# Performance work log

Measured on AMD Instinct MI355X. Metric: run time of the kernel, lower is better.

The kernel has to match this reference:

```python
import jax, jax.numpy as jnp
import numpy as np

B, N, D, C = 32, 8192, 256, 1000  # batch, nodes, dim (dim_original == dim_attention), num_class


def setup_inputs() -> dict:
    key = jax.random.key(0)
    ks = jax.random.split(key, 6)
    s = 1.0 / np.sqrt(D)
    return {
        "atom": jax.random.normal(ks[0], (B, N, D), dtype=jnp.float32),
        "obj": jax.random.normal(ks[1], (B, D), dtype=jnp.float32),
        "W": jax.random.uniform(ks[2], (D, D), jnp.float32, -s, s),        # nn.Linear(D, D, bias=False).weight
        "A": jax.random.uniform(ks[3], (1, 2 * D), jnp.float32, -1.0 / np.sqrt(2 * D), 1.0 / np.sqrt(2 * D)),  # nn.Linear(2D, 1, bias=False).weight
        "CW": jax.random.uniform(ks[4], (C, 2 * D), jnp.float32, -1.0 / np.sqrt(2 * D), 1.0 / np.sqrt(2 * D)),  # classifier weight
        "CB": jax.random.uniform(ks[5], (C,), jnp.float32, -1.0 / np.sqrt(2 * D), 1.0 / np.sqrt(2 * D)),        # classifier bias
    }


def reference(atom, obj, W, A, CW, CB):
    # a1 = w(atom): [B, N, D]; o1 = w(obj): [B, D]
    a1 = jnp.einsum("bnd,kd->bnk", atom, W)
    o1 = obj @ W.T
    # att = Linear_a(cat(a1, broadcast(o1)))  == a1 @ A1 + o1 @ A2 (no concat materialized)
    A1, A2 = A[0, :D], A[0, D:]
    att = a1 @ A1 + (o1 @ A2)[:, None]          # [B, N] attention scores (no softmax)
    # message_a2o = att_weights.bmm(a1).squeeze(): [B, D]
    msg = jnp.einsum("bn,bnd->bd", att, a1)
    # inte == 'concat': classifier(cat(o1, msg))
    preds = jnp.concatenate([o1, msg], axis=-1) @ CW.T + CB  # [B, C]
    return preds
```

## Files before the change

### kernel.cpp

```cpp
#include <hip/hip_runtime.h>

#define DD 256
#define BB 32
#define NN 8192
#define CC 1000
#define SUBS 32
#define CACHED_B 16

typedef float f4 __attribute__((ext_vector_type(4)));

__device__ __forceinline__ f4 ntload(const float* p) {
    return __builtin_nontemporal_load((const f4*)p);
}

template <int CTRL>
__device__ __forceinline__ float dpp_ror_add(float s) {
    int r = __builtin_amdgcn_update_dpp(0, __float_as_int(s), CTRL, 0xF, 0xF, true);
    return s + __int_as_float(r);
}
__device__ __forceinline__ float rowsum16(float s) {
    s = dpp_ror_add<0x121>(s);
    s = dpp_ror_add<0x122>(s);
    s = dpp_ror_add<0x124>(s);
    s = dpp_ror_add<0x128>(s);
    return s;
}

__global__ __launch_bounds__(256) void k_prep(const float* __restrict__ W,
                                              const float* __restrict__ A,
                                              const float* __restrict__ obj,
                                              float* __restrict__ v1,
                                              float* __restrict__ c) {
    int b = blockIdx.x, t = threadIdx.x;
    int q  = t >> 6;
    int cs = (t & 63) * 4;
    __shared__ float s1[4][DD], s2[4][DD];
    __shared__ float sc[4];
    f4 a1 = {0.f, 0.f, 0.f, 0.f}, a2 = a1;
#pragma unroll 8
    for (int k = q; k < DD; k += 4) {
        f4 w = *(const f4*)(W + (size_t)k * DD + cs);
        a1 += A[k] * w;
        a2 += A[DD + k] * w;
    }
    *(f4*)&s1[q][cs] = a1;
    *(f4*)&s2[q][cs] = a2;
    __syncthreads();
    float vv1 = s1[0][t] + s1[1][t] + s1[2][t] + s1[3][t];
    float vv2 = s2[0][t] + s2[1][t] + s2[2][t] + s2[3][t];
    if (b == 0) v1[t] = vv1;
    float p = vv2 * obj[(size_t)b * DD + t];
    p = rowsum16(p);
    p += __shfl_xor(p, 16, 64);
    p += __shfl_xor(p, 32, 64);
    if ((t & 63) == 0) sc[t >> 6] = p;
    __syncthreads();
    if (t == 0) c[b] = sc[0] + sc[1] + sc[2] + sc[3];
}

template <bool NT>
__device__ __forceinline__ void atom_loop(const float* __restrict__ p,
                                          const float4& w0, const float4& w1,
                                          const float4& w2, const float4& w3,
                                          float cb,
                                          f4& A0, f4& A1, f4& A2, f4& A3) {
#pragma unroll 4
    for (int g = 0; g < 16; ++g) {
        f4 x0 = NT ? ntload(p)       : *(const f4*)(p);
        f4 x1 = NT ? ntload(p + 64)  : *(const f4*)(p + 64);
        f4 x2 = NT ? ntload(p + 128) : *(const f4*)(p + 128);
        f4 x3 = NT ? ntload(p + 192) : *(const f4*)(p + 192);
        p += 4 * DD;
        float dot = x0.x * w0.x + x0.y * w0.y + x0.z * w0.z + x0.w * w0.w
                  + x1.x * w1.x + x1.y * w1.y + x1.z * w1.z + x1.w * w1.w
                  + x2.x * w2.x + x2.y * w2.y + x2.z * w2.z + x2.w * w2.w
                  + x3.x * w3.x + x3.y * w3.y + x3.z * w3.z + x3.w * w3.w;
        float att = rowsum16(dot) + cb;
        A0 += att * x0;
        A1 += att * x1;
        A2 += att * x2;
        A3 += att * x3;
    }
}

__global__ __launch_bounds__(256, 4) void k_main(const float* __restrict__ atom,
                                                 const float* __restrict__ v1,
                                                 const float* __restrict__ c,
                                                 float* __restrict__ partials) {
    int blk  = blockIdx.x;
    int b    = blk >> 5;
    int sub  = blk & 31;
    int tid  = threadIdx.x;
    int wave = tid >> 6, lane = tid & 63;
    int grp  = lane >> 4, gl = lane & 15;

    __shared__ float sv1[DD];
    __shared__ float tsh[4][DD];
    sv1[tid] = v1[tid];
    __syncthreads();
    float4 w0 = *(const float4*)&sv1[gl * 4];
    float4 w1 = *(const float4*)&sv1[gl * 4 + 64];
    float4 w2 = *(const float4*)&sv1[gl * 4 + 128];
    float4 w3 = *(const float4*)&sv1[gl * 4 + 192];
    float  cb = c[b];

    const float* p = atom + ((size_t)b * NN + (size_t)sub * 256 + wave * 64 + grp) * DD
                   + gl * 4;

    f4 A0 = {0.f, 0.f, 0.f, 0.f}, A1 = A0, A2 = A0, A3 = A0;

    if (b < CACHED_B) {
        atom_loop<false>(p, w0, w1, w2, w3, cb, A0, A1, A2, A3);
    } else {
        atom_loop<true >(p, w0, w1, w2, w3, cb, A0, A1, A2, A3);
    }

#define XRED(v)                              \
    v.x += __shfl_xor(v.x, 16, 64); v.x += __shfl_xor(v.x, 32, 64); \
    v.y += __shfl_xor(v.y, 16, 64); v.y += __shfl_xor(v.y, 32, 64); \
    v.z += __shfl_xor(v.z, 16, 64); v.z += __shfl_xor(v.z, 32, 64); \
    v.w += __shfl_xor(v.w, 16, 64); v.w += __shfl_xor(v.w, 32, 64);
    XRED(A0) XRED(A1) XRED(A2) XRED(A3)
#undef XRED

    if (grp == 0) {
        *(f4*)&tsh[wave][gl * 4]       = A0;
        *(f4*)&tsh[wave][gl * 4 + 64]  = A1;
        *(f4*)&tsh[wave][gl * 4 + 128] = A2;
        *(f4*)&tsh[wave][gl * 4 + 192] = A3;
    }
    __syncthreads();
    partials[(size_t)blk * DD + tid] =
        tsh[0][tid] + tsh[1][tid] + tsh[2][tid] + tsh[3][tid];
}

__global__ __launch_bounds__(256) void k_mid(const float* __restrict__ partials,
                                             const float* __restrict__ W,
                                             const float* __restrict__ obj,
                                             float* __restrict__ x) {
    int b = blockIdx.x >> 4, q = blockIdx.x & 15;
    int t = threadIdx.x;
    __shared__ float tt[DD];
    __shared__ float so[DD];

    float s = 0.f;
#pragma unroll 8
    for (int i = 0; i < SUBS; ++i) s += partials[((size_t)(b * SUBS + i)) * DD + t];
    tt[t] = s;
    so[t] = obj[(size_t)b * DD + t];
    __syncthreads();

    int kk = t >> 4, cs = t & 15;
    int k  = q * 16 + kk;
    const float4* wr = (const float4*)(W + (size_t)k * DD + cs * 16);
    float p = 0.f, po = 0.f;
#pragma unroll
    for (int ii = 0; ii < 4; ++ii) {
        int i = (ii + cs) & 3;
        float4 a  = wr[i];
        float4 xx = *(const float4*)&tt[cs * 16 + i * 4];
        float4 oo = *(const float4*)&so[cs * 16 + i * 4];
        p  += a.x * xx.x + a.y * xx.y + a.z * xx.z + a.w * xx.w;
        po += a.x * oo.x + a.y * oo.y + a.z * oo.z + a.w * oo.w;
    }
    p  = rowsum16(p);
    po = rowsum16(po);
    if (cs == 0) {
        x[b * 2 * DD + DD + k] = p;
        x[b * 2 * DD + k]      = po;
    }
}

__global__ __launch_bounds__(256) void k_class(const float* __restrict__ x,
                                               const float* __restrict__ CW,
                                               const float* __restrict__ CB,
                                               float* __restrict__ out) {
    int bg = blockIdx.x / 63, ch = blockIdx.x % 63;
    int t = threadIdx.x;
    __shared__ float xs[8][2 * DD];

    {
        const f4* src = (const f4*)(x + (size_t)bg * 8 * 2 * DD);
        f4* dst = (f4*)&xs[0][0];
#pragma unroll
        for (int i = 0; i < 4; ++i) dst[t + 256 * i] = src[t + 256 * i];
    }
    __syncthreads();

    int cl = t >> 4, seg = t & 15;
    int j = ch * 16 + cl;
    if (j < CC) {
        const f4* cw = (const f4*)(CW + (size_t)j * 2 * DD + seg * 32);
        float p[8];
#pragma unroll
        for (int bb = 0; bb < 8; ++bb) p[bb] = 0.f;
#pragma unroll
        for (int ii = 0; ii < 8; ++ii) {
            int i = (ii + seg) & 7;
            f4 a = cw[i];
#pragma unroll
            for (int bb = 0; bb < 8; ++bb) {
                f4 v = *(const f4*)&xs[bb][seg * 32 + i * 4];
                p[bb] += a.x * v.x + a.y * v.y + a.z * v.z + a.w * v.w;
            }
        }
#pragma unroll
        for (int bb = 0; bb < 8; ++bb) p[bb] = rowsum16(p[bb]);
        if (seg == 0) {
            float cb = CB[j];
            int b0 = bg * 8;
#pragma unroll
            for (int bb = 0; bb < 8; ++bb)
                out[(size_t)(b0 + bb) * CC + j] = p[bb] + cb;
        }
    }
}

extern "C" void kernel_launch(void* const* d_in, const int* in_sizes, int n_in,
                              void* d_out, int out_size, void* d_ws, size_t ws_size,
                              hipStream_t stream) {
    const float* atom = (const float*)d_in[0];
    const float* obj  = (const float*)d_in[1];
    const float* W    = (const float*)d_in[2];
    const float* A    = (const float*)d_in[3];
    const float* CW   = (const float*)d_in[4];
    const float* CB   = (const float*)d_in[5];
    float* out = (float*)d_out;

    float* ws = (float*)d_ws;
    float* v1       = ws;
    float* c        = ws + 256;
    float* x        = ws + 512;
    float* partials = x + (size_t)BB * 2 * DD;

    hipLaunchKernelGGL(k_prep,  dim3(BB),        dim3(256), 0, stream, W, A, obj, v1, c);
    hipLaunchKernelGGL(k_main,  dim3(BB * SUBS), dim3(256), 0, stream, atom, v1, c, partials);
    hipLaunchKernelGGL(k_mid,   dim3(BB * 16),   dim3(256), 0, stream, partials, W, obj, x);
    hipLaunchKernelGGL(k_class, dim3(4 * 63),    dim3(256), 0, stream, x, CW, CB, out);
}
```

Before: 66.76 us.

## Fuse mid projection and classifier kernels using an atomic grid barrier

Merges the k_mid and k_class kernels into one launch. After the projection phase, blocks increment a global counter, and the first 252 blocks spin until all 512 blocks have arrived before running the classifier. This removes one kernel launch and its inter-kernel gap. The risk is a deadlock if not all 512 blocks are co-resident, though that is likely fine on this GPU, and the spin-wait adds some polling overhead. The counter is reset in k_prep.

After: 126.2 us. +89.0%, slower.

```diff
diff --git a/kernel.cpp b/kernel.cpp
--- a/kernel.cpp
+++ b/kernel.cpp
@@ -30,8 +30,10 @@
                                               const float* __restrict__ A,
                                               const float* __restrict__ obj,
                                               float* __restrict__ v1,
-                                              float* __restrict__ c) {
+                                              float* __restrict__ c,
+                                              int* __restrict__ done) {
     int b = blockIdx.x, t = threadIdx.x;
+    if (b == 0 && t == 0) *done = 0;
     int q  = t >> 6;
     int cs = (t & 63) * 4;
     __shared__ float s1[4][DD], s2[4][DD];
@@ -134,84 +136,100 @@
         tsh[0][tid] + tsh[1][tid] + tsh[2][tid] + tsh[3][tid];
 }
 
-__global__ __launch_bounds__(256) void k_mid(const float* __restrict__ partials,
-                                             const float* __restrict__ W,
-                                             const float* __restrict__ obj,
-                                             float* __restrict__ x) {
-    int b = blockIdx.x >> 4, q = blockIdx.x & 15;
-    int t = threadIdx.x;
-    __shared__ float tt[DD];
-    __shared__ float so[DD];
-
-    float s = 0.f;
+__global__ __launch_bounds__(256) void k_mc(const float* __restrict__ partials,
+                                            const float* __restrict__ W,
+                                            const float* __restrict__ obj,
+                                            const float* __restrict__ CW,
+                                            const float* __restrict__ CB,
+                                            float* __restrict__ x,
+                                            float* __restrict__ out,
+                                            int* __restrict__ done) {
+    int blk = blockIdx.x, t = threadIdx.x;
+    __shared__ float smem[8 * 2 * DD];
+
+    {
+        int b = blk >> 4, q = blk & 15;
+        float* tt = smem;
+        float* so = smem + DD;
+
+        float s = 0.f;
 #pragma unroll 8
-    for (int i = 0; i < SUBS; ++i) s += partials[((size_t)(b * SUBS + i)) * DD + t];
-    tt[t] = s;
-    so[t] = obj[(size_t)b * DD + t];
-    __syncthreads();
-
-    int kk = t >> 4, cs = t & 15;
-    int k  = q * 16 + kk;
-    const float4* wr = (const float4*)(W + (size_t)k * DD + cs * 16);
-    float p = 0.f, po = 0.f;
-#pragma unroll
-    for (int ii = 0; ii < 4; ++ii) {
-        int i = (ii + cs) & 3;
-        float4 a  = wr[i];
-        float4 xx = *(const float4*)&tt[cs * 16 + i * 4];
-        float4 oo = *(const float4*)&so[cs * 16 + i * 4];
-        p  += a.x * xx.x + a.y * xx.y + a.z * xx.z + a.w * xx.w;
-        po += a.x * oo.x + a.y * oo.y + a.z * oo.z + a.w * oo.w;
-    }
-    p  = rowsum16(p);
-    po = rowsum16(po);
-    if (cs == 0) {
-        x[b * 2 * DD + DD + k] = p;
-        x[b * 2 * DD + k]      = po;
-    }
-}
-
-__global__ __launch_bounds__(256) void k_class(const float* __restrict__ x,
-                                               const float* __restrict__ CW,
-                                               const float* __restrict__ CB,
-                                               float* __restrict__ out) {
-    int bg = blockIdx.x / 63, ch = blockIdx.x % 63;
-    int t = threadIdx.x;
-    __shared__ float xs[8][2 * DD];
+        for (int i = 0; i < SUBS; ++i)
+            s += partials[((size_t)(b * SUBS + i)) * DD + t];
+        tt[t] = s;
+        so[t] = obj[(size_t)b * DD + t];
+        __syncthreads();
+
+        int kk = t >> 4, cs = t & 15;
+        int k  = q * 16 + kk;
+        const float4* wr = (const float4*)(W + (size_t)k * DD + cs * 16);
+        float p = 0.f, po = 0.f;
+#pragma unroll
+        for (int ii = 0; ii < 4; ++ii) {
+            int i = (ii + cs) & 3;
+            float4 a  = wr[i];
+            float4 xx = *(const float4*)&tt[cs * 16 + i * 4];
+            float4 oo = *(const float4*)&so[cs * 16 + i * 4];
+            p  += a.x * xx.x + a.y * xx.y + a.z * xx.z + a.w * xx.w;
+            po += a.x * oo.x + a.y * oo.y + a.z * oo.z + a.w * oo.w;
+        }
+        p  = rowsum16(p);
+        po = rowsum16(po);
+        if (cs == 0) {
+            x[b * 2 * DD + DD + k] = p;
+            x[b * 2 * DD + k]      = po;
+        }
+    }
+
+    __threadfence();
+    __syncthreads();
+    if (t == 0) __hip_atomic_fetch_add(done, 1, __ATOMIC_RELEASE,
+                                       __HIP_MEMORY_SCOPE_AGENT);
+    if (blk >= 252) return;
+    if (t == 0) {
+        while (__hip_atomic_load(done, __ATOMIC_ACQUIRE,
+                                 __HIP_MEMORY_SCOPE_AGENT) < 512)
+            __builtin_amdgcn_s_sleep(8);
+    }
+    __syncthreads();
+    __threadfence();
 
     {
+        int bg = blk / 63, ch = blk % 63;
+        float (*xs)[2 * DD] = (float (*)[2 * DD])smem;
+
         const f4* src = (const f4*)(x + (size_t)bg * 8 * 2 * DD);
         f4* dst = (f4*)&xs[0][0];
 #pragma unroll
         for (int i = 0; i < 4; ++i) dst[t + 256 * i] = src[t + 256 * i];
-    }
-    __syncthreads();
-
-    int cl = t >> 4, seg = t & 15;
-    int j = ch * 16 + cl;
-    if (j < CC) {
-        const f4* cw = (const f4*)(CW + (size_t)j * 2 * DD + seg * 32);
-        float p[8];
-#pragma unroll
-        for (int bb = 0; bb < 8; ++bb) p[bb] = 0.f;
-#pragma unroll
-        for (int ii = 0; ii < 8; ++ii) {
-            int i = (ii + seg) & 7;
-            f4 a = cw[i];
-#pragma unroll
-            for (int bb = 0; bb < 8; ++bb) {
-                f4 v = *(const f4*)&xs[bb][seg * 32 + i * 4];
-                p[bb] += a.x * v.x + a.y * v.y + a.z * v.z + a.w * v.w;
+        __syncthreads();
+
+        int cl = t >> 4, seg = t & 15;
+        int j = ch * 16 + cl;
+        if (j < CC) {
+            const f4* cw = (const f4*)(CW + (size_t)j * 2 * DD + seg * 32);
+            float p[8];
+#pragma unroll
+            for (int bb = 0; bb < 8; ++bb) p[bb] = 0.f;
+#pragma unroll
+            for (int ii = 0; ii < 8; ++ii) {
+                int i = (ii + seg) & 7;
+                f4 a = cw[i];
+#pragma unroll
+                for (int bb = 0; bb < 8; ++bb) {
+                    f4 v = *(const f4*)&xs[bb][seg * 32 + i * 4];
+                    p[bb] += a.x * v.x + a.y * v.y + a.z * v.z + a.w * v.w;
+                }
             }
-        }
-#pragma unroll
-        for (int bb = 0; bb < 8; ++bb) p[bb] = rowsum16(p[bb]);
-        if (seg == 0) {
-            float cb = CB[j];
-            int b0 = bg * 8;
-#pragma unroll
-            for (int bb = 0; bb < 8; ++bb)
-                out[(size_t)(b0 + bb) * CC + j] = p[bb] + cb;
+#pragma unroll
+            for (int bb = 0; bb < 8; ++bb) p[bb] = rowsum16(p[bb]);
+            if (seg == 0) {
+                float cb = CB[j];
+                int b0 = bg * 8;
+#pragma unroll
+                for (int bb = 0; bb < 8; ++bb)
+                    out[(size_t)(b0 + bb) * CC + j] = p[bb] + cb;
+            }
         }
     }
 }
@@ -232,9 +250,10 @@
     float* c        = ws + 256;
     float* x        = ws + 512;
     float* partials = x + (size_t)BB * 2 * DD;
-
-    hipLaunchKernelGGL(k_prep,  dim3(BB),        dim3(256), 0, stream, W, A, obj, v1, c);
-    hipLaunchKernelGGL(k_main,  dim3(BB * SUBS), dim3(256), 0, stream, atom, v1, c, partials);
-    hipLaunchKernelGGL(k_mid,   dim3(BB * 16),   dim3(256), 0, stream, partials, W, obj, x);
-    hipLaunchKernelGGL(k_class, dim3(4 * 63),    dim3(256), 0, stream, x, CW, CB, out);
-}
+    int*   done     = (int*)(partials + (size_t)BB * SUBS * DD);
+
+    hipLaunchKernelGGL(k_prep, dim3(BB),        dim3(256), 0, stream, W, A, obj, v1, c, done);
+    hipLaunchKernelGGL(k_main, dim3(BB * SUBS), dim3(256), 0, stream, atom, v1, c, partials);
+    hipLaunchKernelGGL(k_mc,   dim3(BB * 16),   dim3(256), 0, stream,
+                       partials, W, obj, CW, CB, x, out, done);
+}
```

## Fuse mid projection and classifier into one kernel; compute o1 in prep

Applied to the files above, without the earlier changes.

Moves the obj@W^T projection (o1) into k_prep, which already streams W. k_mid and k_class become a single k_fin kernel that reduces the partials, projects msg through W and runs the classifier slice. This cuts one kernel launch and the round trip of x through global memory between the stages. In exchange, each of the 256 k_fin blocks recomputes the full 256x256 W projection for its batch row (redundant 8x per batch), and classifier weights are no longer reused across 8 batches per block, so CW traffic rises.

After: 87.73 us. 1.31x slower.

```diff
diff --git a/kernel.cpp b/kernel.cpp
--- a/kernel.cpp
+++ b/kernel.cpp
@@ -30,18 +30,26 @@
                                               const float* __restrict__ A,
                                               const float* __restrict__ obj,
                                               float* __restrict__ v1,
-                                              float* __restrict__ c) {
+                                              float* __restrict__ c,
+                                              float* __restrict__ x) {
     int b = blockIdx.x, t = threadIdx.x;
-    int q  = t >> 6;
-    int cs = (t & 63) * 4;
+    int q    = t >> 6;
+    int lane = t & 63;
+    int cs   = lane * 4;
     __shared__ float s1[4][DD], s2[4][DD];
     __shared__ float sc[4];
     f4 a1 = {0.f, 0.f, 0.f, 0.f}, a2 = a1;
-#pragma unroll 8
+    f4 ob = *(const f4*)(obj + (size_t)b * DD + cs);
+#pragma unroll 4
     for (int k = q; k < DD; k += 4) {
         f4 w = *(const f4*)(W + (size_t)k * DD + cs);
         a1 += A[k] * w;
         a2 += A[DD + k] * w;
+        float po = ob.x * w.x + ob.y * w.y + ob.z * w.z + ob.w * w.w;
+        po = rowsum16(po);
+        po += __shfl_xor(po, 16, 64);
+        po += __shfl_xor(po, 32, 64);
+        if (lane == 0) x[b * 2 * DD + k] = po;
     }
     *(f4*)&s1[q][cs] = a1;
     *(f4*)&s2[q][cs] = a2;
@@ -134,84 +142,61 @@
         tsh[0][tid] + tsh[1][tid] + tsh[2][tid] + tsh[3][tid];
 }
 
-__global__ __launch_bounds__(256) void k_mid(const float* __restrict__ partials,
+__global__ __launch_bounds__(256) void k_fin(const float* __restrict__ partials,
                                              const float* __restrict__ W,
-                                             const float* __restrict__ obj,
-                                             float* __restrict__ x) {
-    int b = blockIdx.x >> 4, q = blockIdx.x & 15;
+                                             const float* __restrict__ x,
+                                             const float* __restrict__ CW,
+                                             const float* __restrict__ CB,
+                                             float* __restrict__ out) {
+    int blk = blockIdx.x;
+    int b = blk >> 3, cc = blk & 7;
     int t = threadIdx.x;
+    __shared__ float xcat[2 * DD];
     __shared__ float tt[DD];
-    __shared__ float so[DD];
 
     float s = 0.f;
 #pragma unroll 8
-    for (int i = 0; i < SUBS; ++i) s += partials[((size_t)(b * SUBS + i)) * DD + t];
-    tt[t] = s;
-    so[t] = obj[(size_t)b * DD + t];
+    for (int i = 0; i < SUBS; ++i)
+        s += partials[((size_t)(b * SUBS + i)) * DD + t];
+    tt[t]   = s;
+    xcat[t] = x[b * 2 * DD + t];
     __syncthreads();
 
     int kk = t >> 4, cs = t & 15;
-    int k  = q * 16 + kk;
-    const float4* wr = (const float4*)(W + (size_t)k * DD + cs * 16);
-    float p = 0.f, po = 0.f;
+#pragma unroll 4
+    for (int qq = 0; qq < 16; ++qq) {
+        int k = qq * 16 + kk;
+        const float4* wr = (const float4*)(W + (size_t)k * DD + cs * 16);
+        float p = 0.f;
 #pragma unroll
-    for (int ii = 0; ii < 4; ++ii) {
-        int i = (ii + cs) & 3;
-        float4 a  = wr[i];
-        float4 xx = *(const float4*)&tt[cs * 16 + i * 4];
-        float4 oo = *(const float4*)&so[cs * 16 + i * 4];
-        p  += a.x * xx.x + a.y * xx.y + a.z * xx.z + a.w * xx.w;
-        po += a.x * oo.x + a.y * oo.y + a.z * oo.z + a.w * oo.w;
-    }
-    p  = rowsum16(p);
-    po = rowsum16(po);
-    if (cs == 0) {
-        x[b * 2 * DD + DD + k] = p;
-        x[b * 2 * DD + k]      = po;
-    }
-}
-
-__global__ __launch_bounds__(256) void k_class(const float* __restrict__ x,
-                                               const float* __restrict__ CW,
-                                               const float* __restrict__ CB,
-                                               float* __restrict__ out) {
-    int bg = blockIdx.x / 63, ch = blockIdx.x % 63;
-    int t = threadIdx.x;
-    __shared__ float xs[8][2 * DD];
-
-    {
-        const f4* src = (const f4*)(x + (size_t)bg * 8 * 2 * DD);
-        f4* dst = (f4*)&xs[0][0];
+        for (int ii = 0; ii < 4; ++ii) {
+            int i = (ii + cs) & 3;
+            float4 a  = wr[i];
+            float4 xx = *(const float4*)&tt[cs * 16 + i * 4];
+            p += a.x * xx.x + a.y * xx.y + a.z * xx.z + a.w * xx.w;
+        }
+        p = rowsum16(p);
+        if (cs == 0) xcat[DD + k] = p;
+    }
+    __syncthreads();
+
+    int cl = t >> 4, seg = t & 15;
+#pragma unroll 2
+    for (int pp = 0; pp < 8; ++pp) {
+        int jj = pp * 16 + cl;
+        if (jj < 125) {
+            int j = cc * 125 + jj;
+            const f4* cw = (const f4*)(CW + (size_t)j * 2 * DD + seg * 32);
+            float p = 0.f;
 #pragma unroll
-        for (int i = 0; i < 4; ++i) dst[t + 256 * i] = src[t + 256 * i];
-    }
-    __syncthreads();
-
-    int cl = t >> 4, seg = t & 15;
-    int j = ch * 16 + cl;
-    if (j < CC) {
-        const f4* cw = (const f4*)(CW + (size_t)j * 2 * DD + seg * 32);
-        float p[8];
-#pragma unroll
-        for (int bb = 0; bb < 8; ++bb) p[bb] = 0.f;
-#pragma unroll
-        for (int ii = 0; ii < 8; ++ii) {
-            int i = (ii + seg) & 7;
-            f4 a = cw[i];
-#pragma unroll
-            for (int bb = 0; bb < 8; ++bb) {
-                f4 v = *(const f4*)&xs[bb][seg * 32 + i * 4];
-                p[bb] += a.x * v.x + a.y * v.y + a.z * v.z + a.w * v.w;
+            for (int ii = 0; ii < 8; ++ii) {
+                int i = (ii + seg) & 7;
+                f4 a = cw[i];
+                f4 v = *(const f4*)&xcat[seg * 32 + i * 4];
+                p += a.x * v.x + a.y * v.y + a.z * v.z + a.w * v.w;
             }
-        }
-#pragma unroll
-        for (int bb = 0; bb < 8; ++bb) p[bb] = rowsum16(p[bb]);
-        if (seg == 0) {
-            float cb = CB[j];
-            int b0 = bg * 8;
-#pragma unroll
-            for (int bb = 0; bb < 8; ++bb)
-                out[(size_t)(b0 + bb) * CC + j] = p[bb] + cb;
+            p = rowsum16(p);
+            if (seg == 0) out[(size_t)b * CC + j] = p + CB[j];
         }
     }
 }
@@ -233,8 +218,8 @@
     float* x        = ws + 512;
     float* partials = x + (size_t)BB * 2 * DD;
 
-    hipLaunchKernelGGL(k_prep,  dim3(BB),        dim3(256), 0, stream, W, A, obj, v1, c);
-    hipLaunchKernelGGL(k_main,  dim3(BB * SUBS), dim3(256), 0, stream, atom, v1, c, partials);
-    hipLaunchKernelGGL(k_mid,   dim3(BB * 16),   dim3(256), 0, stream, partials, W, obj, x);
-    hipLaunchKernelGGL(k_class, dim3(4 * 63),    dim3(256), 0, stream, x, CW, CB, out);
-}
+    hipLaunchKernelGGL(k_prep, dim3(BB),        dim3(256), 0, stream, W, A, obj, v1, c, x);
+    hipLaunchKernelGGL(k_main, dim3(BB * SUBS), dim3(256), 0, stream, atom, v1, c, partials);
+    hipLaunchKernelGGL(k_fin,  dim3(BB * 8),    dim3(256), 0, stream,
+                       partials, W, x, CW, CB, out);
+}
```
